# Kernel optimization log

Measured on AMD Instinct MI355X. Metric: run time of the kernel, lower is better.

The kernel has to match this reference:

```python
import jax, jax.numpy as jnp
import numpy as np

EMBED_DIM = 256
NUM_HEADS = 8
NUM_QUERIES = 448
TEMPERATURE = 10000.0
SCALE = 100.0
EPS = 1e-5
B, N = 1, 512
NUM_CLASSES = 91


def box_rel_encoding(src_boxes, tgt_boxes, eps=EPS):
    # boxes: [B, N, 4] as (cx, cy, w, h)
    xy1, wh1 = src_boxes[..., :2], src_boxes[..., 2:]
    xy2, wh2 = tgt_boxes[..., :2], tgt_boxes[..., 2:]
    delta_xy = jnp.abs(xy1[..., :, None, :] - xy2[..., None, :, :])          # [B,N,N,2]
    delta_xy = jnp.log(delta_xy / (wh1[..., :, None, :] + eps) + 1.0)
    delta_wh = jnp.log((wh1[..., :, None, :] + eps) / (wh2[..., None, :, :] + eps))
    return jnp.concatenate([delta_xy, delta_wh], axis=-1)                    # [B,N,N,4]


def get_sine_pos_embed(pos, num_pos_feats, temperature=TEMPERATURE, scale=SCALE):
    # pos: [..., C]; returns [..., C * num_pos_feats]; exchange_xy=False
    dim_t = jnp.arange(num_pos_feats, dtype=pos.dtype)
    dim_t = temperature ** (2.0 * jnp.floor(dim_t / 2.0) / num_pos_feats)
    x = pos[..., None] * scale / dim_t                                        # [...,C,F]
    emb = jnp.stack([jnp.sin(x[..., 0::2]), jnp.cos(x[..., 1::2])], axis=-1)  # [...,C,F/2,2]
    emb = emb.reshape(x.shape)                                                # [...,C,F]
    return emb.reshape(pos.shape[:-1] + (pos.shape[-1] * num_pos_feats,))


def setup_inputs() -> dict:
    key = jax.random.key(0)
    ks = jax.random.split(key, 9)
    s = 0.02
    return {
        "src_boxes": jax.random.uniform(ks[0], (B, N, 4), jnp.float32, 0.05, 0.95),
        "pred_logits": jax.random.normal(ks[1], (B, N, NUM_CLASSES), jnp.float32),
        "rank_emb": jax.random.normal(ks[2], (NUM_QUERIES, EMBED_DIM), jnp.float32) * s,
        "pre_W": jax.random.normal(ks[3], (EMBED_DIM, EMBED_DIM), jnp.float32) * s,
        "pre_b": jax.random.normal(ks[4], (EMBED_DIM,), jnp.float32) * s,
        "post_W": jax.random.normal(ks[5], (EMBED_DIM, 2 * EMBED_DIM), jnp.float32) * s,
        "post_b": jax.random.normal(ks[6], (EMBED_DIM,), jnp.float32) * s,
        "attn_W": jax.random.normal(ks[7], (NUM_HEADS, EMBED_DIM), jnp.float32) * s,
        "attn_b": jax.random.normal(ks[8], (NUM_HEADS,), jnp.float32) * s,
        "layer_idx": 2,
    }


def reference(src_boxes, pred_logits, rank_emb, pre_W, pre_b, post_W, post_b, attn_W, attn_b, layer_idx):
    num_denoising = N - NUM_QUERIES
    # --- no-grad block: pairwise box relation + rank-ordered gather reorder ---
    base = box_rel_encoding(src_boxes, src_boxes)                            # [B,N,N,4]
    scores = jnp.max(jax.nn.sigmoid(pred_logits[:, num_denoising:]), axis=-1)  # [B,Q]
    order = jnp.argsort(-scores, axis=1)                                      # descending  [B,Q]
    rank_indices = jnp.broadcast_to(jnp.arange(N, dtype=order.dtype), (B, N))
    rank_indices = rank_indices.at[:, num_denoising:].set(order + num_denoising)
    nr = base[:, num_denoising:, num_denoising:]                              # [B,Q,Q,4]
    nr = jnp.take_along_axis(nr, order[:, :, None, None], axis=1)
    nr = jnp.take_along_axis(nr, order[:, None, :, None], axis=2)
    base = base.at[:, num_denoising:, num_denoising:].set(nr)
    base = jax.lax.stop_gradient(base)
    # --- sine positional embedding of relation: [B,N,N,EMBED_DIM] ---
    pos = get_sine_pos_embed(base, EMBED_DIM // 4)
    # --- rank-aware relation: embedding -> pre linear -> pairwise sum ---
    normal_rank = rank_emb @ pre_W.T + pre_b                                  # [Q,E]
    rank_rel = jnp.zeros((B, N, EMBED_DIM), src_boxes.dtype)
    rank_rel = rank_rel.at[:, num_denoising:].set(normal_rank[None])
    rank_rel = rank_rel[:, :, None, :] + rank_rel[:, None, :, :]              # [B,N,N,E]
    relation = jnp.concatenate([pos, rank_rel], axis=-1)                      # [B,N,N,2E]
    relation = relation @ post_W.T + post_b                                   # [B,N,N,E]
    attn = jax.nn.relu(relation @ attn_W.T + attn_b)                          # [B,N,N,H]
    attn = jnp.transpose(attn, (0, 3, 1, 2))                                  # [B,H,N,N]
    return attn, rank_indices
```

## Files before the change

kernel.cpp:

```cpp
#include <hip/hip_runtime.h>
#include <hip/hip_bf16.h>
#include <math.h>

#define NN 512
#define NQ 448
#define ND 64
#define NC 91
#define ED 256
#define NH 8

typedef __attribute__((ext_vector_type(8))) short bf16x8;
typedef __attribute__((ext_vector_type(4))) float f32x4;

struct FreqArg { float fr[32]; };

__device__ int   g_perm[NN];
__device__ float g_c0[NH];
__device__ float g_afull[NN * NH];
__device__ float g_part[64 * 512];
__device__ float g_scores[NQ];
__device__ float g_nr[NQ * ED];
__device__ __align__(16) unsigned short g_WB[8 * 64 * 8];

__device__ inline unsigned short f2bfbits(float x) {
    __hip_bfloat16 h = __float2bfloat16(x);
    union { __hip_bfloat16 b; unsigned short u; } cv; cv.b = h; return cv.u;
}

__global__ __launch_bounds__(512) void precomp1(const float* __restrict__ logits,
                                                const float* __restrict__ attn_W,
                                                const float* __restrict__ attn_b,
                                                const float* __restrict__ post_W,
                                                const float* __restrict__ post_b,
                                                const float* __restrict__ pre_W,
                                                const float* __restrict__ pre_b,
                                                const float* __restrict__ rank_emb) {
    __shared__ float smem[48 * 257];
    int bid = blockIdx.x;
    int t = threadIdx.x;
    if (bid < 64) {
        int h = bid >> 3, cc = bid & 7;
        float* sAW = smem;
        if (t < 32) sAW[t] = attn_W[h * ED + cc * 32 + t];
        __syncthreads();
        float m = 0.f;
        const float* pw = post_W + (size_t)(cc * 32) * 512 + t;
#pragma unroll
        for (int ci = 0; ci < 32; ++ci) m = fmaf(sAW[ci], pw[(size_t)ci * 512], m);
        g_part[(size_t)bid * 512 + t] = m;
    } else if (bid < 72) {
        int W = (bid - 64) * 8 + (t >> 6);
        int lane = t & 63;
        for (int qi = 0; qi < 7; ++qi) {
            int q = W * 7 + qi;
            const float* row = logits + (size_t)(ND + q) * NC;
            float m = (lane < NC) ? row[lane] : -INFINITY;
            int c2 = lane + 64;
            if (c2 < NC) m = fmaxf(m, row[c2]);
            for (int off = 32; off > 0; off >>= 1) m = fmaxf(m, __shfl_down(m, off, 64));
            if (lane == 0) g_scores[q] = m;
        }
    } else if (bid == 72) {
        int h = t >> 6, lane = t & 63;
        float v = 0.f;
#pragma unroll
        for (int k = 0; k < 4; ++k) {
            int c = lane + 64 * k;
            v = fmaf(attn_W[h * ED + c], post_b[c], v);
        }
        for (int off = 32; off > 0; off >>= 1) v += __shfl_down(v, off, 64);
        if (lane == 0) g_c0[h] = attn_b[h] + v;
    } else {
        int nb = bid - 73;
        int q0 = (nb >> 3) * 16, d0 = (nb & 7) * 32;
        float* sP = smem;
        float* sR = smem + 32 * 257;
        for (int v = t; v < 32 * 256; v += 512)
            sP[(v >> 8) * 257 + (v & 255)] = pre_W[(size_t)(d0 + (v >> 8)) * ED + (v & 255)];
        for (int v = t; v < 16 * 256; v += 512)
            sR[(v >> 8) * 257 + (v & 255)] = rank_emb[(size_t)(q0 + (v >> 8)) * ED + (v & 255)];
        __syncthreads();
        int q = t >> 5, dl = t & 31;
        float acc = pre_b[d0 + dl];
#pragma unroll 8
        for (int e = 0; e < 256; ++e) acc = fmaf(sR[q * 257 + e], sP[dl * 257 + e], acc);
        g_nr[(size_t)(q0 + q) * ED + d0 + dl] = acc;
    }
}

__global__ __launch_bounds__(256) void precomp2(float* __restrict__ out2) {
    int bid = blockIdx.x;
    int t = threadIdx.x;
    if (bid < 56) {
        __shared__ float sW[NH * 260];
        __shared__ float sN[NH * 260];
        int q0 = bid * 8;
        for (int v = t; v < 2048; v += 256) {
            int h = v >> 8, d = v & 255;
            float s = 0.f;
#pragma unroll
            for (int cc = 0; cc < 8; ++cc) s += g_part[(size_t)(h * 8 + cc) * 512 + 256 + d];
            sW[h * 260 + d] = s;
        }
        for (int v = t; v < 2048; v += 256)
            sN[(v >> 8) * 260 + (v & 255)] = g_nr[(size_t)(q0 + (v >> 8)) * ED + (v & 255)];
        __syncthreads();
        int o = t >> 2, sub = t & 3;
        int q = o >> 3, h = o & 7;
        float a = 0.f;
#pragma unroll 8
        for (int e2 = 0; e2 < 64; ++e2) {
            int e = sub + 4 * e2;
            a = fmaf(sN[q * 260 + e], sW[h * 260 + e], a);
        }
        a += __shfl_xor(a, 1, 64);
        a += __shfl_xor(a, 2, 64);
        if (sub == 0) g_afull[(size_t)(ND + q0 + q) * NH + h] = a;
    } else if (bid < 58) {
        for (int vv = t; vv < 2048; vv += 256) {
            int v = (bid - 56) * 2048 + vv;
            int s = v >> 9;
            int lane = (v >> 3) & 63;
            int ii = v & 7;
            int g = lane >> 4, hh = lane & 15;
            int k = s * 4 + (ii >> 1), r = ii & 1;
            int d = g * 64 + 2 * k + r;
            float w = 0.f;
            if (hh < NH) {
#pragma unroll
                for (int cc = 0; cc < 8; ++cc) w += g_part[(size_t)(hh * 8 + cc) * 512 + d];
            }
            g_WB[v] = f2bfbits(w);
        }
    } else {
        __shared__ float sc[NQ];
        for (int v = t; v < NQ; v += 256) sc[v] = g_scores[v];
        __syncthreads();
        int q1 = t, q2 = t + 256;
        float s1 = sc[q1];
        float s2 = (q2 < NQ) ? sc[q2] : 0.f;
        int r1 = 0, r2 = 0;
        for (int j = 0; j < NQ; ++j) {
            float sj = sc[j];
            r1 += ((sj > s1) || (sj == s1 && j < q1)) ? 1 : 0;
            r2 += ((sj > s2) || (sj == s2 && j < q2)) ? 1 : 0;
        }
        g_perm[ND + r1] = ND + q1;
        out2[ND + r1] = (float)(ND + q1);
        if (q2 < NQ) {
            g_perm[ND + r2] = ND + q2;
            out2[ND + r2] = (float)(ND + q2);
        }
        if (t < ND) {
            g_perm[t] = t;
            out2[t] = (float)t;
            for (int h = 0; h < NH; ++h) g_afull[t * NH + h] = 0.f;
        }
    }
}

__global__ __launch_bounds__(256) void relation_main(const float* __restrict__ boxes,
                                                     FreqArg fa,
                                                     float* __restrict__ out) {
    __shared__ bf16x8 sWB[8][64];
    int t = threadIdx.x;
    ((uint4*)sWB)[t]       = ((const uint4*)g_WB)[t];
    ((uint4*)sWB)[t + 256] = ((const uint4*)g_WB)[t + 256];
    __syncthreads();

    int wave = t >> 6, lane = t & 63;
    int g = lane >> 4, r = lane & 15;
    int i = blockIdx.x >> 3;
    int j = ((blockIdx.x & 7) << 6) + (wave << 4) + r;

    int pi = i, pj = j;
    if (i >= ND && j >= ND) { pi = g_perm[i]; pj = g_perm[j]; }
    float4 b1 = ((const float4*)boxes)[pi];
    float4 b2 = ((const float4*)boxes)[pj];
    const float eps = 1e-5f;
    float ft;
    if (g == 0)      ft = logf(fabsf(b1.x - b2.x) / (b1.z + eps) + 1.0f);
    else if (g == 1) ft = logf(fabsf(b1.y - b2.y) / (b1.w + eps) + 1.0f);
    else if (g == 2) ft = logf((b1.z + eps) / (b2.z + eps));
    else             ft = logf((b1.w + eps) / (b2.w + eps));

    f32x4 acc = {0.f, 0.f, 0.f, 0.f};
#pragma unroll
    for (int s = 0; s < 8; ++s) {
        bf16x8 bfrag;
#pragma unroll
        for (int a = 0; a < 4; ++a) {
            float rev = ft * fa.fr[s * 4 + a];
            rev -= floorf(rev);
            float sv = __builtin_amdgcn_sinf(rev);
            float cv = __builtin_amdgcn_cosf(rev);
            bfrag[2 * a]     = (short)f2bfbits(sv);
            bfrag[2 * a + 1] = (short)f2bfbits(cv);
        }
        acc = __builtin_amdgcn_mfma_f32_16x16x32_bf16(sWB[s][lane], bfrag, acc, 0, 0, 0);
    }

    if (g < 2) {
        float4 cb = *(const float4*)(g_c0 + g * 4);
        float4 ai = *(const float4*)(g_afull + i * NH + g * 4);
        float4 aj = *(const float4*)(g_afull + j * NH + g * 4);
        const float* cbp = (const float*)&cb;
        const float* aip = (const float*)&ai;
        const float* ajp = (const float*)&aj;
#pragma unroll
        for (int q = 0; q < 4; ++q) {
            int h = g * 4 + q;
            float v = acc[q] + cbp[q] + aip[q] + ajp[q];
            v = v > 0.f ? v : 0.f;
            out[(size_t)h * (NN * NN) + i * NN + j] = v;
        }
    }
}

extern "C" void kernel_launch(void* const* d_in, const int* in_sizes, int n_in,
                              void* d_out, int out_size, void* d_ws, size_t ws_size,
                              hipStream_t stream) {
    const float* boxes    = (const float*)d_in[0];
    const float* logits   = (const float*)d_in[1];
    const float* rank_emb = (const float*)d_in[2];
    const float* pre_W    = (const float*)d_in[3];
    const float* pre_b    = (const float*)d_in[4];
    const float* post_W   = (const float*)d_in[5];
    const float* post_b   = (const float*)d_in[6];
    const float* attn_W   = (const float*)d_in[7];
    const float* attn_b   = (const float*)d_in[8];
    float* out = (float*)d_out;

    precomp1<<<297, 512, 0, stream>>>(logits, attn_W, attn_b, post_W, post_b,
                                      pre_W, pre_b, rank_emb);
    precomp2<<<59, 256, 0, stream>>>(out + (size_t)NH * NN * NN);

    FreqArg fa;
    for (int k = 0; k < 32; ++k)
        fa.fr[k] = (float)(100.0 / (2.0 * M_PI) / pow(10000.0, (double)k / 32.0));

    relation_main<<<4096, 256, 0, stream>>>(boxes, fa, out);
}
```

Before: 45.02 us.

## Fuse all three kernels into one persistent kernel with grid barriers

Result: slower. 101.3 us (+125.1%).

```diff
diff --git a/kernel.cpp b/kernel.cpp
--- a/kernel.cpp
+++ b/kernel.cpp
@@ -8,6 +8,7 @@
 #define NC 91
 #define ED 256
 #define NH 8
+#define NBLK 256
 
 typedef __attribute__((ext_vector_type(8))) short bf16x8;
 typedef __attribute__((ext_vector_type(4))) float f32x4;
@@ -21,25 +22,51 @@
 __device__ float g_scores[NQ];
 __device__ float g_nr[NQ * ED];
 __device__ __align__(16) unsigned short g_WB[8 * 64 * 8];
+__device__ unsigned g_bar0 = 0, g_bar1 = 0;
 
 __device__ inline unsigned short f2bfbits(float x) {
     __hip_bfloat16 h = __float2bfloat16(x);
     union { __hip_bfloat16 b; unsigned short u; } cv; cv.b = h; return cv.u;
 }
 
-__global__ __launch_bounds__(512) void precomp1(const float* __restrict__ logits,
-                                                const float* __restrict__ attn_W,
-                                                const float* __restrict__ attn_b,
-                                                const float* __restrict__ post_W,
-                                                const float* __restrict__ post_b,
-                                                const float* __restrict__ pre_W,
-                                                const float* __restrict__ pre_b,
-                                                const float* __restrict__ rank_emb) {
-    __shared__ float smem[48 * 257];
-    int bid = blockIdx.x;
-    int t = threadIdx.x;
-    if (bid < 64) {
-        int h = bid >> 3, cc = bid & 7;
+__device__ inline void grid_barrier(unsigned* cnt) {
+    __syncthreads();
+    if (threadIdx.x == 0) {
+        __threadfence();
+        unsigned old = __hip_atomic_fetch_add(cnt, 1u, __ATOMIC_ACQ_REL, __HIP_MEMORY_SCOPE_AGENT);
+        if (old == NBLK - 1) {
+            __hip_atomic_store(cnt, 0u, __ATOMIC_RELEASE, __HIP_MEMORY_SCOPE_AGENT);
+        } else {
+            while (__hip_atomic_load(cnt, __ATOMIC_ACQUIRE, __HIP_MEMORY_SCOPE_AGENT) != 0u)
+                __builtin_amdgcn_s_sleep(2);
+        }
+        __threadfence();
+    }
+    __syncthreads();
+}
+
+__device__ void task_p1(int tk, int t, float* smem,
+                        const float* __restrict__ logits, const float* __restrict__ attn_W,
+                        const float* __restrict__ attn_b, const float* __restrict__ post_W,
+                        const float* __restrict__ post_b, const float* __restrict__ pre_W,
+                        const float* __restrict__ pre_b, const float* __restrict__ rank_emb) {
+    if (tk < 224) {
+        int q0 = (tk >> 3) * 16, d0 = (tk & 7) * 32;
+        float* sP = smem;
+        float* sR = smem + 32 * 257;
+        for (int v = t; v < 32 * 256; v += 512)
+            sP[(v >> 8) * 257 + (v & 255)] = pre_W[(size_t)(d0 + (v >> 8)) * ED + (v & 255)];
+        for (int v = t; v < 16 * 256; v += 512)
+            sR[(v >> 8) * 257 + (v & 255)] = rank_emb[(size_t)(q0 + (v >> 8)) * ED + (v & 255)];
+        __syncthreads();
+        int q = t >> 5, dl = t & 31;
+        float acc = pre_b[d0 + dl];
+#pragma unroll 8
+        for (int e = 0; e < 256; ++e) acc = fmaf(sR[q * 257 + e], sP[dl * 257 + e], acc);
+        g_nr[(size_t)(q0 + q) * ED + d0 + dl] = acc;
+    } else if (tk < 288) {
+        int f = tk - 224;
+        int h = f >> 3, cc = f & 7;
         float* sAW = smem;
         if (t < 32) sAW[t] = attn_W[h * ED + cc * 32 + t];
         __syncthreads();
@@ -47,9 +74,9 @@
         const float* pw = post_W + (size_t)(cc * 32) * 512 + t;
 #pragma unroll
         for (int ci = 0; ci < 32; ++ci) m = fmaf(sAW[ci], pw[(size_t)ci * 512], m);
-        g_part[(size_t)bid * 512 + t] = m;
-    } else if (bid < 72) {
-        int W = (bid - 64) * 8 + (t >> 6);
+        g_part[(size_t)f * 512 + t] = m;
+    } else if (tk < 296) {
+        int W = (tk - 288) * 8 + (t >> 6);
         int lane = t & 63;
         for (int qi = 0; qi < 7; ++qi) {
             int q = W * 7 + qi;
@@ -60,7 +87,7 @@
             for (int off = 32; off > 0; off >>= 1) m = fmaxf(m, __shfl_down(m, off, 64));
             if (lane == 0) g_scores[q] = m;
         }
-    } else if (bid == 72) {
+    } else {
         int h = t >> 6, lane = t & 63;
         float v = 0.f;
 #pragma unroll
@@ -70,54 +97,38 @@
         }
         for (int off = 32; off > 0; off >>= 1) v += __shfl_down(v, off, 64);
         if (lane == 0) g_c0[h] = attn_b[h] + v;
-    } else {
-        int nb = bid - 73;
-        int q0 = (nb >> 3) * 16, d0 = (nb & 7) * 32;
-        float* sP = smem;
-        float* sR = smem + 32 * 257;
-        for (int v = t; v < 32 * 256; v += 512)
-            sP[(v >> 8) * 257 + (v & 255)] = pre_W[(size_t)(d0 + (v >> 8)) * ED + (v & 255)];
-        for (int v = t; v < 16 * 256; v += 512)
-            sR[(v >> 8) * 257 + (v & 255)] = rank_emb[(size_t)(q0 + (v >> 8)) * ED + (v & 255)];
-        __syncthreads();
-        int q = t >> 5, dl = t & 31;
-        float acc = pre_b[d0 + dl];
-#pragma unroll 8
-        for (int e = 0; e < 256; ++e) acc = fmaf(sR[q * 257 + e], sP[dl * 257 + e], acc);
-        g_nr[(size_t)(q0 + q) * ED + d0 + dl] = acc;
-    }
-}
-
-__global__ __launch_bounds__(256) void precomp2(float* __restrict__ out2) {
-    int bid = blockIdx.x;
-    int t = threadIdx.x;
+    }
+}
+
+__device__ void task_p2(int bid, int t, float* smem, float* __restrict__ out2) {
     if (bid < 56) {
-        __shared__ float sW[NH * 260];
-        __shared__ float sN[NH * 260];
+        float* sW = smem;
+        float* sN = smem + 8 * 260;
         int q0 = bid * 8;
-        for (int v = t; v < 2048; v += 256) {
+        for (int v = t; v < 2048; v += 512) {
             int h = v >> 8, d = v & 255;
             float s = 0.f;
 #pragma unroll
             for (int cc = 0; cc < 8; ++cc) s += g_part[(size_t)(h * 8 + cc) * 512 + 256 + d];
             sW[h * 260 + d] = s;
         }
-        for (int v = t; v < 2048; v += 256)
+        for (int v = t; v < 2048; v += 512)
             sN[(v >> 8) * 260 + (v & 255)] = g_nr[(size_t)(q0 + (v >> 8)) * ED + (v & 255)];
         __syncthreads();
-        int o = t >> 2, sub = t & 3;
+        int o = t >> 3, sub = t & 7;
         int q = o >> 3, h = o & 7;
         float a = 0.f;
 #pragma unroll 8
-        for (int e2 = 0; e2 < 64; ++e2) {
-            int e = sub + 4 * e2;
+        for (int e2 = 0; e2 < 32; ++e2) {
+            int e = sub + 8 * e2;
             a = fmaf(sN[q * 260 + e], sW[h * 260 + e], a);
         }
         a += __shfl_xor(a, 1, 64);
         a += __shfl_xor(a, 2, 64);
+        a += __shfl_xor(a, 4, 64);
         if (sub == 0) g_afull[(size_t)(ND + q0 + q) * NH + h] = a;
     } else if (bid < 58) {
-        for (int vv = t; vv < 2048; vv += 256) {
+        for (int vv = t; vv < 2048; vv += 512) {
             int v = (bid - 56) * 2048 + vv;
             int s = v >> 9;
             int lane = (v >> 3) & 63;
@@ -132,24 +143,19 @@
             }
             g_WB[v] = f2bfbits(w);
         }
-    } else {
-        __shared__ float sc[NQ];
-        for (int v = t; v < NQ; v += 256) sc[v] = g_scores[v];
-        __syncthreads();
-        int q1 = t, q2 = t + 256;
-        float s1 = sc[q1];
-        float s2 = (q2 < NQ) ? sc[q2] : 0.f;
-        int r1 = 0, r2 = 0;
-        for (int j = 0; j < NQ; ++j) {
-            float sj = sc[j];
-            r1 += ((sj > s1) || (sj == s1 && j < q1)) ? 1 : 0;
-            r2 += ((sj > s2) || (sj == s2 && j < q2)) ? 1 : 0;
-        }
-        g_perm[ND + r1] = ND + q1;
-        out2[ND + r1] = (float)(ND + q1);
-        if (q2 < NQ) {
-            g_perm[ND + r2] = ND + q2;
-            out2[ND + r2] = (float)(ND + q2);
+    } else if (bid == 58) {
+        float* sc = smem;
+        for (int v = t; v < NQ; v += 512) sc[v] = g_scores[v];
+        __syncthreads();
+        if (t < NQ) {
+            float s1 = sc[t];
+            int r1 = 0;
+            for (int j = 0; j < NQ; ++j) {
+                float sj = sc[j];
+                r1 += ((sj > s1) || (sj == s1 && j < t)) ? 1 : 0;
+            }
+            g_perm[ND + r1] = ND + t;
+            out2[ND + r1] = (float)(ND + t);
         }
         if (t < ND) {
             g_perm[t] = t;
@@ -159,60 +165,92 @@
     }
 }
 
-__global__ __launch_bounds__(256) void relation_main(const float* __restrict__ boxes,
-                                                     FreqArg fa,
-                                                     float* __restrict__ out) {
-    __shared__ bf16x8 sWB[8][64];
+__global__ __launch_bounds__(512) void fused_all(const float* __restrict__ boxes,
+                                                 const float* __restrict__ logits,
+                                                 const float* __restrict__ rank_emb,
+                                                 const float* __restrict__ pre_W,
+                                                 const float* __restrict__ pre_b,
+                                                 const float* __restrict__ post_W,
+                                                 const float* __restrict__ post_b,
+                                                 const float* __restrict__ attn_W,
+                                                 const float* __restrict__ attn_b,
+                                                 FreqArg fa,
+                                                 float* __restrict__ out) {
+    __shared__ __align__(16) float smem[48 * 257];
+    int bid = blockIdx.x;
     int t = threadIdx.x;
-    ((uint4*)sWB)[t]       = ((const uint4*)g_WB)[t];
-    ((uint4*)sWB)[t + 256] = ((const uint4*)g_WB)[t + 256];
+    float* out2 = out + (size_t)NH * NN * NN;
+
+    task_p1(bid, t, smem, logits, attn_W, attn_b, post_W, post_b, pre_W, pre_b, rank_emb);
+    if (bid + 256 < 297) {
+        __syncthreads();
+        task_p1(bid + 256, t, smem, logits, attn_W, attn_b, post_W, post_b, pre_W, pre_b, rank_emb);
+    }
+    grid_barrier(&g_bar0);
+
+    task_p2(bid, t, smem, out2);
+    grid_barrier(&g_bar1);
+
+    ((uint4*)smem)[t] = ((const uint4*)g_WB)[t];
+    int* sPerm = (int*)(smem + 2048);
+    sPerm[t] = g_perm[t];
+    float* sAf = smem + 2560;
+    for (int v = t; v < NN * NH; v += 512) sAf[v] = g_afull[v];
     __syncthreads();
 
-    int wave = t >> 6, lane = t & 63;
+    const bf16x8* sWB = (const bf16x8*)smem;
+    int wv = t >> 6, lane = t & 63;
     int g = lane >> 4, r = lane & 15;
-    int i = blockIdx.x >> 3;
-    int j = ((blockIdx.x & 7) << 6) + (wave << 4) + r;
-
-    int pi = i, pj = j;
-    if (i >= ND && j >= ND) { pi = g_perm[i]; pj = g_perm[j]; }
-    float4 b1 = ((const float4*)boxes)[pi];
-    float4 b2 = ((const float4*)boxes)[pj];
+    int i = 2 * bid + (wv >> 2);
+    int q4 = wv & 3;
+
+    float4 b1p = ((const float4*)boxes)[i];
+    float4 b1s = b1p;
+    if (i >= ND) b1s = ((const float4*)boxes)[sPerm[i]];
+    const float* cb = g_c0 + g * 4;
+    const float* ai_pl = sAf + i * NH + g * 4;
     const float eps = 1e-5f;
-    float ft;
-    if (g == 0)      ft = logf(fabsf(b1.x - b2.x) / (b1.z + eps) + 1.0f);
-    else if (g == 1) ft = logf(fabsf(b1.y - b2.y) / (b1.w + eps) + 1.0f);
-    else if (g == 2) ft = logf((b1.z + eps) / (b2.z + eps));
-    else             ft = logf((b1.w + eps) / (b2.w + eps));
-
-    f32x4 acc = {0.f, 0.f, 0.f, 0.f};
-#pragma unroll
-    for (int s = 0; s < 8; ++s) {
-        bf16x8 bfrag;
-#pragma unroll
-        for (int a = 0; a < 4; ++a) {
-            float rev = ft * fa.fr[s * 4 + a];
-            rev -= floorf(rev);
-            float sv = __builtin_amdgcn_sinf(rev);
-            float cv = __builtin_amdgcn_cosf(rev);
-            bfrag[2 * a]     = (short)f2bfbits(sv);
-            bfrag[2 * a + 1] = (short)f2bfbits(cv);
-        }
-        acc = __builtin_amdgcn_mfma_f32_16x16x32_bf16(sWB[s][lane], bfrag, acc, 0, 0, 0);
-    }
-
-    if (g < 2) {
-        float4 cb = *(const float4*)(g_c0 + g * 4);
-        float4 ai = *(const float4*)(g_afull + i * NH + g * 4);
-        float4 aj = *(const float4*)(g_afull + j * NH + g * 4);
-        const float* cbp = (const float*)&cb;
-        const float* aip = (const float*)&ai;
-        const float* ajp = (const float*)&aj;
-#pragma unroll
-        for (int q = 0; q < 4; ++q) {
-            int h = g * 4 + q;
-            float v = acc[q] + cbp[q] + aip[q] + ajp[q];
-            v = v > 0.f ? v : 0.f;
-            out[(size_t)h * (NN * NN) + i * NN + j] = v;
+
+#pragma unroll
+    for (int k = 0; k < 8; ++k) {
+        int j0 = q4 * 128 + k * 16;
+        int j = j0 + r;
+        bool prm = (i >= ND) && (j0 >= ND);
+        float4 b1 = prm ? b1s : b1p;
+        int pj = prm ? sPerm[j] : j;
+        float4 b2 = ((const float4*)boxes)[pj];
+
+        float ft;
+        if (g == 0)      ft = logf(fabsf(b1.x - b2.x) / (b1.z + eps) + 1.0f);
+        else if (g == 1) ft = logf(fabsf(b1.y - b2.y) / (b1.w + eps) + 1.0f);
+        else if (g == 2) ft = logf((b1.z + eps) / (b2.z + eps));
+        else             ft = logf((b1.w + eps) / (b2.w + eps));
+
+        f32x4 acc = {0.f, 0.f, 0.f, 0.f};
+#pragma unroll
+        for (int s = 0; s < 8; ++s) {
+            bf16x8 bfrag;
+#pragma unroll
+            for (int a = 0; a < 4; ++a) {
+                float rev = ft * fa.fr[s * 4 + a];
+                rev -= floorf(rev);
+                float sv = __builtin_amdgcn_sinf(rev);
+                float cv = __builtin_amdgcn_cosf(rev);
+                bfrag[2 * a]     = (short)f2bfbits(sv);
+                bfrag[2 * a + 1] = (short)f2bfbits(cv);
+            }
+            acc = __builtin_amdgcn_mfma_f32_16x16x32_bf16(sWB[s * 64 + lane], bfrag, acc, 0, 0, 0);
+        }
+
+        if (g < 2) {
+            const float* aj = sAf + j * NH + g * 4;
+#pragma unroll
+            for (int qq = 0; qq < 4; ++qq) {
+                int h = g * 4 + qq;
+                float v = acc[qq] + cb[qq] + ai_pl[qq] + aj[qq];
+                v = v > 0.f ? v : 0.f;
+                out[(size_t)h * (NN * NN) + i * NN + j] = v;
+            }
         }
     }
 }
@@ -231,13 +269,10 @@
     const float* attn_b   = (const float*)d_in[8];
     float* out = (float*)d_out;
 
-    precomp1<<<297, 512, 0, stream>>>(logits, attn_W, attn_b, post_W, post_b,
-                                      pre_W, pre_b, rank_emb);
-    precomp2<<<59, 256, 0, stream>>>(out + (size_t)NH * NN * NN);
-
     FreqArg fa;
     for (int k = 0; k < 32; ++k)
         fa.fr[k] = (float)(100.0 / (2.0 * M_PI) / pow(10000.0, (double)k / 32.0));
 
-    relation_main<<<4096, 256, 0, stream>>>(boxes, fa, out);
-}
+    fused_all<<<NBLK, 512, 0, stream>>>(boxes, logits, rank_emb, pre_W, pre_b,
+                                        post_W, post_b, attn_W, attn_b, fa, out);
+}
```

## Merge precompute kernels into one and reassociate rank projection through folded weights

Applied to the files above, without the earlier changes.

After: 51.03 us. +13.4%, slower.

```diff
diff --git a/kernel.cpp b/kernel.cpp
--- a/kernel.cpp
+++ b/kernel.cpp
@@ -17,9 +17,6 @@
 __device__ int   g_perm[NN];
 __device__ float g_c0[NH];
 __device__ float g_afull[NN * NH];
-__device__ float g_part[64 * 512];
-__device__ float g_scores[NQ];
-__device__ float g_nr[NQ * ED];
 __device__ __align__(16) unsigned short g_WB[8 * 64 * 8];
 
 __device__ inline unsigned short f2bfbits(float x) {
@@ -27,134 +24,111 @@
     union { __hip_bfloat16 b; unsigned short u; } cv; cv.b = h; return cv.u;
 }
 
-__global__ __launch_bounds__(512) void precomp1(const float* __restrict__ logits,
-                                                const float* __restrict__ attn_W,
-                                                const float* __restrict__ attn_b,
-                                                const float* __restrict__ post_W,
-                                                const float* __restrict__ post_b,
-                                                const float* __restrict__ pre_W,
-                                                const float* __restrict__ pre_b,
-                                                const float* __restrict__ rank_emb) {
-    __shared__ float smem[48 * 257];
-    int bid = blockIdx.x;
-    int t = threadIdx.x;
-    if (bid < 64) {
-        int h = bid >> 3, cc = bid & 7;
-        float* sAW = smem;
-        if (t < 32) sAW[t] = attn_W[h * ED + cc * 32 + t];
-        __syncthreads();
+__global__ __launch_bounds__(512) void precomp(const float* __restrict__ logits,
+                                               const float* __restrict__ attn_W,
+                                               const float* __restrict__ attn_b,
+                                               const float* __restrict__ post_W,
+                                               const float* __restrict__ post_b,
+                                               const float* __restrict__ pre_W,
+                                               const float* __restrict__ pre_b,
+                                               const float* __restrict__ rank_emb,
+                                               float* __restrict__ out2) {
+    __shared__ float sAW[ED];
+    __shared__ float sFold[512];
+    __shared__ float sU2[512];
+    __shared__ float sU[ED];
+    __shared__ float sc[NQ];
+    __shared__ float sB2a;
+    int bid = blockIdx.x, t = threadIdx.x;
+
+    if (bid < NH) {
+        int h = bid;
+        if (t < ED) sAW[t] = attn_W[h * ED + t];
+        __syncthreads();
+
         float m = 0.f;
-        const float* pw = post_W + (size_t)(cc * 32) * 512 + t;
-#pragma unroll
-        for (int ci = 0; ci < 32; ++ci) m = fmaf(sAW[ci], pw[(size_t)ci * 512], m);
-        g_part[(size_t)bid * 512 + t] = m;
-    } else if (bid < 72) {
-        int W = (bid - 64) * 8 + (t >> 6);
-        int lane = t & 63;
-        for (int qi = 0; qi < 7; ++qi) {
-            int q = W * 7 + qi;
+        const float* pw = post_W + t;
+#pragma unroll 16
+        for (int c = 0; c < ED; ++c) m = fmaf(sAW[c], pw[(size_t)c * 512], m);
+        sFold[t] = m;
+        __syncthreads();
+
+        {
+            int e = t & 255, half = t >> 8;
+            float acc = 0.f;
+            const float* pwc = pre_W + (size_t)(half * 128) * ED + e;
+#pragma unroll 16
+            for (int dl = 0; dl < 128; ++dl)
+                acc = fmaf(sFold[256 + half * 128 + dl], pwc[(size_t)dl * ED], acc);
+            sU2[half * 256 + e] = acc;
+        }
+        if (t < 64) {
+            float v = 0.f;
+#pragma unroll
+            for (int k = 0; k < 4; ++k) v = fmaf(sAW[t + 64 * k], post_b[t + 64 * k], v);
+            for (int off = 32; off > 0; off >>= 1) v += __shfl_down(v, off, 64);
+            if (t == 0) g_c0[h] = attn_b[h] + v;
+        } else if (t < 128) {
+            int l = t - 64;
+            float v = 0.f;
+#pragma unroll
+            for (int k = 0; k < 4; ++k) v = fmaf(sFold[256 + l + 64 * k], pre_b[l + 64 * k], v);
+            for (int off = 32; off > 0; off >>= 1) v += __shfl_down(v, off, 64);
+            if (l == 0) sB2a = v;
+        }
+        if (t < 256) {
+            int s = t >> 5, g = (t >> 3) & 3, ii = t & 7;
+            int d = g * 64 + ((s * 4 + (ii >> 1)) << 1) + (ii & 1);
+            g_WB[s * 512 + (g * 16 + h) * 8 + ii] = f2bfbits(sFold[d]);
+        }
+        if (t < ND) g_afull[t * NH + h] = 0.f;
+        __syncthreads();
+        if (t < ED) sU[t] = sU2[t] + sU2[256 + t];
+        __syncthreads();
+
+        float b2a = sB2a;
+        for (int pass = 0; pass < 14; ++pass) {
+            int q = pass * 32 + (t >> 4);
+            int sub = t & 15;
+            const float* re = rank_emb + (size_t)q * ED;
+            float a = 0.f;
+#pragma unroll
+            for (int kk = 0; kk < 16; ++kk) a = fmaf(re[sub + 16 * kk], sU[sub + 16 * kk], a);
+            a += __shfl_xor(a, 1, 64);
+            a += __shfl_xor(a, 2, 64);
+            a += __shfl_xor(a, 4, 64);
+            a += __shfl_xor(a, 8, 64);
+            if (sub == 0) g_afull[(size_t)(ND + q) * NH + h] = b2a + a;
+        }
+    } else {
+        for (int v = t; v < 4096; v += 512) {
+            int lane = (v >> 3) & 63;
+            if ((lane & 15) >= NH) g_WB[v] = 0;
+        }
+        int W = t >> 6, lane = t & 63;
+        for (int qi = 0; qi < 56; ++qi) {
+            int q = W * 56 + qi;
             const float* row = logits + (size_t)(ND + q) * NC;
             float m = (lane < NC) ? row[lane] : -INFINITY;
             int c2 = lane + 64;
             if (c2 < NC) m = fmaxf(m, row[c2]);
             for (int off = 32; off > 0; off >>= 1) m = fmaxf(m, __shfl_down(m, off, 64));
-            if (lane == 0) g_scores[q] = m;
-        }
-    } else if (bid == 72) {
-        int h = t >> 6, lane = t & 63;
-        float v = 0.f;
-#pragma unroll
-        for (int k = 0; k < 4; ++k) {
-            int c = lane + 64 * k;
-            v = fmaf(attn_W[h * ED + c], post_b[c], v);
-        }
-        for (int off = 32; off > 0; off >>= 1) v += __shfl_down(v, off, 64);
-        if (lane == 0) g_c0[h] = attn_b[h] + v;
-    } else {
-        int nb = bid - 73;
-        int q0 = (nb >> 3) * 16, d0 = (nb & 7) * 32;
-        float* sP = smem;
-        float* sR = smem + 32 * 257;
-        for (int v = t; v < 32 * 256; v += 512)
-            sP[(v >> 8) * 257 + (v & 255)] = pre_W[(size_t)(d0 + (v >> 8)) * ED + (v & 255)];
-        for (int v = t; v < 16 * 256; v += 512)
-            sR[(v >> 8) * 257 + (v & 255)] = rank_emb[(size_t)(q0 + (v >> 8)) * ED + (v & 255)];
-        __syncthreads();
-        int q = t >> 5, dl = t & 31;
-        float acc = pre_b[d0 + dl];
-#pragma unroll 8
-        for (int e = 0; e < 256; ++e) acc = fmaf(sR[q * 257 + e], sP[dl * 257 + e], acc);
-        g_nr[(size_t)(q0 + q) * ED + d0 + dl] = acc;
-    }
-}
-
-__global__ __launch_bounds__(256) void precomp2(float* __restrict__ out2) {
-    int bid = blockIdx.x;
-    int t = threadIdx.x;
-    if (bid < 56) {
-        __shared__ float sW[NH * 260];
-        __shared__ float sN[NH * 260];
-        int q0 = bid * 8;
-        for (int v = t; v < 2048; v += 256) {
-            int h = v >> 8, d = v & 255;
-            float s = 0.f;
-#pragma unroll
-            for (int cc = 0; cc < 8; ++cc) s += g_part[(size_t)(h * 8 + cc) * 512 + 256 + d];
-            sW[h * 260 + d] = s;
-        }
-        for (int v = t; v < 2048; v += 256)
-            sN[(v >> 8) * 260 + (v & 255)] = g_nr[(size_t)(q0 + (v >> 8)) * ED + (v & 255)];
-        __syncthreads();
-        int o = t >> 2, sub = t & 3;
-        int q = o >> 3, h = o & 7;
-        float a = 0.f;
-#pragma unroll 8
-        for (int e2 = 0; e2 < 64; ++e2) {
-            int e = sub + 4 * e2;
-            a = fmaf(sN[q * 260 + e], sW[h * 260 + e], a);
-        }
-        a += __shfl_xor(a, 1, 64);
-        a += __shfl_xor(a, 2, 64);
-        if (sub == 0) g_afull[(size_t)(ND + q0 + q) * NH + h] = a;
-    } else if (bid < 58) {
-        for (int vv = t; vv < 2048; vv += 256) {
-            int v = (bid - 56) * 2048 + vv;
-            int s = v >> 9;
-            int lane = (v >> 3) & 63;
-            int ii = v & 7;
-            int g = lane >> 4, hh = lane & 15;
-            int k = s * 4 + (ii >> 1), r = ii & 1;
-            int d = g * 64 + 2 * k + r;
-            float w = 0.f;
-            if (hh < NH) {
-#pragma unroll
-                for (int cc = 0; cc < 8; ++cc) w += g_part[(size_t)(hh * 8 + cc) * 512 + d];
+            if (lane == 0) sc[q] = m;
+        }
+        __syncthreads();
+        if (t < NQ) {
+            float s1 = sc[t];
+            int r1 = 0;
+            for (int j = 0; j < NQ; ++j) {
+                float sj = sc[j];
+                r1 += ((sj > s1) || (sj == s1 && j < t)) ? 1 : 0;
             }
-            g_WB[v] = f2bfbits(w);
-        }
-    } else {
-        __shared__ float sc[NQ];
-        for (int v = t; v < NQ; v += 256) sc[v] = g_scores[v];
-        __syncthreads();
-        int q1 = t, q2 = t + 256;
-        float s1 = sc[q1];
-        float s2 = (q2 < NQ) ? sc[q2] : 0.f;
-        int r1 = 0, r2 = 0;
-        for (int j = 0; j < NQ; ++j) {
-            float sj = sc[j];
-            r1 += ((sj > s1) || (sj == s1 && j < q1)) ? 1 : 0;
-            r2 += ((sj > s2) || (sj == s2 && j < q2)) ? 1 : 0;
-        }
-        g_perm[ND + r1] = ND + q1;
-        out2[ND + r1] = (float)(ND + q1);
-        if (q2 < NQ) {
-            g_perm[ND + r2] = ND + q2;
-            out2[ND + r2] = (float)(ND + q2);
+            g_perm[ND + r1] = ND + t;
+            out2[ND + r1] = (float)(ND + t);
         }
         if (t < ND) {
             g_perm[t] = t;
             out2[t] = (float)t;
-            for (int h = 0; h < NH; ++h) g_afull[t * NH + h] = 0.f;
         }
     }
 }
@@ -231,9 +205,9 @@
     const float* attn_b   = (const float*)d_in[8];
     float* out = (float*)d_out;
 
-    precomp1<<<297, 512, 0, stream>>>(logits, attn_W, attn_b, post_W, post_b,
-                                      pre_W, pre_b, rank_emb);
-    precomp2<<<59, 256, 0, stream>>>(out + (size_t)NH * NN * NN);
+    precomp<<<NH + 1, 512, 0, stream>>>(logits, attn_W, attn_b, post_W, post_b,
+                                        pre_W, pre_b, rank_emb,
+                                        out + (size_t)NH * NN * NN);
 
     FreqArg fa;
     for (int k = 0; k < 32; ++k)
```
